# Kernel optimization log

Hardware: AMD Instinct MI355X
Metric: run time of the kernel (lower is better)

Reference implementation:

```python
import jax, jax.numpy as jnp
import numpy as np

B, T, N, E = 64, 500, 21, 210
IN_DIM, HID, OUT_DIM = 1, 128, 1


def gcn_norm(edge_index, edge_weight, num_nodes):
    # PyG gcn_norm: add self loops (weight 1), deg over target nodes, symmetric normalization.
    src, dst = edge_index[0], edge_index[1]
    loop = jnp.arange(num_nodes)
    src = jnp.concatenate([src, loop])
    dst = jnp.concatenate([dst, loop])
    ew = jnp.concatenate([edge_weight, jnp.ones((num_nodes,), edge_weight.dtype)])
    deg = jnp.zeros((num_nodes,), edge_weight.dtype).at[dst].add(ew)
    dinv = jnp.where(deg > 0, deg ** -0.5, 0.0)
    norm = dinv[src] * ew * dinv[dst]
    # Dense N x N (N=21, tiny) normalized adjacency; out[i] = sum_j A[i, j] x[j].
    return jnp.zeros((num_nodes, num_nodes), edge_weight.dtype).at[dst, src].add(norm)


def _forward(edge_index, x, edge_weight, Wz_1, bz_1, lzw_1, lzb_1, Wr_1, br_1, lrw_1, lrb_1, Wh_1, bh_1, lhw_1, lhb_1, Wz_2, bz_2, lzw_2, lzb_2, Wr_2, br_2, lrw_2, lrb_2, Wh_2, bh_2, lhw_2, lhb_2, cls_w, cls_b):
    A = gcn_norm(edge_index, edge_weight, N)

    def gcn(X, W, b):  # X: (B, N, F)
        return jnp.einsum("ij,bjf->bif", A, X @ W) + b

    def cell(X, H, Wz, bz, lzw, lzb, Wr, br, lrw, lrb, Wh, bh, lhw, lhb):
        Z = jax.nn.sigmoid(jnp.concatenate([gcn(X, Wz, bz), H], -1) @ lzw + lzb)
        R = jax.nn.sigmoid(jnp.concatenate([gcn(X, Wr, br), H], -1) @ lrw + lrb)
        Ht = jnp.tanh(jnp.concatenate([gcn(X, Wh, bh), H * R], -1) @ lhw + lhb)
        return Z * H + (1.0 - Z) * Ht

    def step(carry, x_t):  # x_t: (B, N)
        H1, H2 = carry
        X = x_t[..., None]  # (B, N, 1)
        H1 = cell(X, H1, Wz_1, bz_1, lzw_1, lzb_1, Wr_1, br_1, lrw_1, lrb_1, Wh_1, bh_1, lhw_1, lhb_1)
        H2 = cell(H1, H2, Wz_2, bz_2, lzw_2, lzb_2, Wr_2, br_2, lrw_2, lrb_2, Wh_2, bh_2, lhw_2, lhb_2)
        return (H1, H2), H2.mean(axis=1)  # mean over nodes -> (B, HID)

    H0 = jnp.zeros((x.shape[0], N, HID), x.dtype)
    _, outs = jax.lax.scan(step, (H0, H0), jnp.moveaxis(x, 1, 0))  # outs: (T, B, HID)
    seq_out = outs.mean(axis=0)  # mean over time (== mean over nodes then time in original)
    return seq_out @ cls_w + cls_b  # (B, OUT_DIM)


def setup_inputs():
    key = jax.random.key(0)
    ks = list(jax.random.split(key, 20))
    kit = iter(ks)

    def nrm(shape, scale=0.05):
        return jax.random.normal(next(kit), shape, jnp.float32) * scale

    inp = {}
    inp["x"] = jax.random.normal(next(kit), (B, T, N), jnp.float32)
    inp["edge_index"] = jax.random.randint(next(kit), (2, E), 0, N)
    inp["edge_weight"] = jax.random.uniform(next(kit), (E,), jnp.float32)
    for tag, in_dim in (("1", IN_DIM), ("2", HID)):
        for g in "zrh":
            inp[f"W{g}_{tag}"] = nrm((in_dim, HID))
            inp[f"b{g}_{tag}"] = jnp.zeros((HID,), jnp.float32)
            inp[f"l{g}w_{tag}"] = nrm((2 * HID, HID))
            inp[f"l{g}b_{tag}"] = jnp.zeros((HID,), jnp.float32)
    inp["cls_w"] = nrm((HID, OUT_DIM))
    inp["cls_b"] = jnp.zeros((OUT_DIM,), jnp.float32)
    return inp


def reference(x, edge_index, edge_weight, Wz_1, bz_1, lzw_1, lzb_1, Wr_1, br_1, lrw_1, lrb_1, Wh_1, bh_1, lhw_1, lhb_1, Wz_2, bz_2, lzw_2, lzb_2, Wr_2, br_2, lrw_2, lrb_2, Wh_2, bh_2, lhw_2, lhb_2, cls_w, cls_b):
    return _forward(edge_index, x, edge_weight, Wz_1, bz_1, lzw_1, lzb_1, Wr_1, br_1, lrw_1, lrb_1, Wh_1, bh_1, lhw_1, lhb_1, Wz_2, bz_2, lzw_2, lzb_2, Wr_2, br_2, lrw_2, lrb_2, Wh_2, bh_2, lhw_2, lhb_2, cls_w, cls_b)
```

## Files before the change

kernel.cpp:

```cpp
#include <hip/hip_runtime.h>
#include <hip/hip_bf16.h>


#define NN 21
#define NROW 24
#define HID 128
#define TSTEPS 500
#define EDGES 210
#define RPT 6

#define WS_A     0
#define WS_VEC   1600
#define WS_LZR1  3200
#define WS_LH1   36000
#define WS_WE2   52400
#define WS_LZR2  101600
#define WS_LH2   134400
#define WS_FLAGS 150784
#define WS_RING  154880
#define RING_SLOT 3072
#define WS_END   (WS_RING + 64 * 2 * RING_SLOT)

#define WAVE_SYNC() asm volatile("s_waitcnt lgkmcnt(0)" ::: "memory")
#define VM_SYNC()   asm volatile("s_waitcnt vmcnt(0)" ::: "memory")

typedef float v2f __attribute__((ext_vector_type(2)));

__device__ __forceinline__ v2f lo2(float4 w) { v2f v = {w.x, w.y}; return v; }
__device__ __forceinline__ v2f hi2(float4 w) { v2f v = {w.z, w.w}; return v; }
__device__ __forceinline__ void pkf(v2f& acc, float s, v2f w) {
    v2f ss = {s, s};
    acc = __builtin_elementwise_fma(ss, w, acc);
}
__device__ __forceinline__ float sigmoidf(float v) {
    return 1.0f / (1.0f + expf(-v));
}
__device__ __forceinline__ void dc_store(float* p, float v) {
    asm volatile("global_store_dword %0, %1, off sc0 sc1" :: "v"(p), "v"(v) : "memory");
}

__global__ void build_A(const int* __restrict__ ei, const float* __restrict__ ew,
                        float* __restrict__ Aout) {
    __shared__ double deg[NN];
    __shared__ double dinv[NN];
    __shared__ double Asm[NN * NN];
    int t = threadIdx.x;
    for (int k = t; k < NN * NN; k += blockDim.x) Asm[k] = 0.0;
    if (t < NN) deg[t] = 1.0;
    __syncthreads();
    if (t == 0) {
        for (int e = 0; e < EDGES; e++) deg[ei[EDGES + e]] += (double)ew[e];
        for (int i = 0; i < NN; i++) dinv[i] = deg[i] > 0.0 ? 1.0 / sqrt(deg[i]) : 0.0;
        for (int e = 0; e < EDGES; e++) {
            int s = ei[e], d = ei[EDGES + e];
            Asm[d * NN + s] += dinv[s] * (double)ew[e] * dinv[d];
        }
        for (int i = 0; i < NN; i++) Asm[i * NN + i] += dinv[i] * dinv[i];
    }
    __syncthreads();
    for (int k = t; k < NROW * NN; k += blockDim.x)
        Aout[k] = (k < NN * NN) ? (float)Asm[k] : 0.0f;
}

__global__ void init_flags(unsigned* f) {
    int i = blockIdx.x * blockDim.x + threadIdx.x;
    if (i < 4096) f[i] = 0u;
}

__global__ void pack_bot(const float* __restrict__ w0, const float* __restrict__ w1,
                         float4* __restrict__ out, int ngate) {
    int t = blockIdx.x * blockDim.x + threadIdx.x;
    int per_c = ngate * 128;
    int total = 32 * per_c;
    if (t >= total) return;
    int c = t / per_c, rem = t - c * per_c;
    int gate = rem >> 7;
    int r2 = rem & 127;
    int k2 = r2 >> 6;
    int f0 = r2 & 63;
    int k = 4 * c + 2 * k2;
    const float* src = (gate == 0) ? w0 : w1;
    float4 v;
    v.x = src[(128 + k) * 128 + f0];
    v.y = src[(128 + k) * 128 + f0 + 64];
    v.z = src[(128 + k + 1) * 128 + f0];
    v.w = src[(128 + k + 1) * 128 + f0 + 64];
    out[t] = v;
}

__global__ void make_weff2(const float* __restrict__ Wz2, const float* __restrict__ Wr2,
                           const float* __restrict__ Wh2,
                           const float* __restrict__ lzw2, const float* __restrict__ lrw2,
                           const float* __restrict__ lhw2,
                           float4* __restrict__ out) {
    int t = blockIdx.x * blockDim.x + threadIdx.x;
    if (t >= 32 * 384) return;
    int c = t / 384, rem = t - c * 384;
    int g = rem >> 7;
    int r2 = rem & 127;
    int k2 = r2 >> 6;
    int f0 = r2 & 63;
    int k = 4 * c + 2 * k2;
    const float* W = (g == 0) ? Wz2 : (g == 1) ? Wr2 : Wh2;
    const float* L = (g == 0) ? lzw2 : (g == 1) ? lrw2 : lhw2;
    double a0 = 0, a1 = 0, a2 = 0, a3 = 0;
    for (int m = 0; m < 128; m++) {
        double w0 = (double)W[k * 128 + m];
        double w1 = (double)W[(k + 1) * 128 + m];
        a0 += w0 * (double)L[m * 128 + f0];
        a1 += w0 * (double)L[m * 128 + f0 + 64];
        a2 += w1 * (double)L[m * 128 + f0];
        a3 += w1 * (double)L[m * 128 + f0 + 64];
    }
    out[t] = make_float4((float)a0, (float)a1, (float)a2, (float)a3);
}

__global__ void make_vecs(const float* __restrict__ Wz1, const float* __restrict__ Wr1,
                          const float* __restrict__ Wh1,
                          const float* __restrict__ bz1, const float* __restrict__ br1,
                          const float* __restrict__ bh1,
                          const float* __restrict__ lzw1, const float* __restrict__ lrw1,
                          const float* __restrict__ lhw1,
                          const float* __restrict__ lzb1, const float* __restrict__ lrb1,
                          const float* __restrict__ lhb1,
                          const float* __restrict__ bz2, const float* __restrict__ br2,
                          const float* __restrict__ bh2,
                          const float* __restrict__ lzw2, const float* __restrict__ lrw2,
                          const float* __restrict__ lhw2,
                          const float* __restrict__ lzb2, const float* __restrict__ lrb2,
                          const float* __restrict__ lhb2,
                          float* __restrict__ out) {
    int t = blockIdx.x * blockDim.x + threadIdx.x;
    if (t >= 9 * 128) return;
    int v = t >> 7, f = t & 127;
    double acc = 0.0;
    if (v < 3) {
        const float* W = (v == 0) ? Wz1 : (v == 1) ? Wr1 : Wh1;
        const float* L = (v == 0) ? lzw1 : (v == 1) ? lrw1 : lhw1;
        for (int m = 0; m < 128; m++) acc += (double)W[m] * (double)L[m * 128 + f];
    } else if (v < 6) {
        int g = v - 3;
        const float* bb = (g == 0) ? bz1 : (g == 1) ? br1 : bh1;
        const float* L  = (g == 0) ? lzw1 : (g == 1) ? lrw1 : lhw1;
        const float* lb = (g == 0) ? lzb1 : (g == 1) ? lrb1 : lhb1;
        for (int m = 0; m < 128; m++) acc += (double)bb[m] * (double)L[m * 128 + f];
        acc += (double)lb[f];
    } else {
        int g = v - 6;
        const float* bb = (g == 0) ? bz2 : (g == 1) ? br2 : bh2;
        const float* L  = (g == 0) ? lzw2 : (g == 1) ? lrw2 : lhw2;
        const float* lb = (g == 0) ? lzb2 : (g == 1) ? lrb2 : lhb2;
        for (int m = 0; m < 128; m++) acc += (double)bb[m] * (double)L[m * 128 + f];
        acc += (double)lb[f];
    }
    out[t] = (float)acc;
}

__global__ __launch_bounds__(256, 1) void tgcn_split(
    const float* __restrict__ x, float* __restrict__ ws,
    const float* __restrict__ cls_w, const float* __restrict__ cls_b,
    float* __restrict__ out)
{
    const int bid = blockIdx.x;
    const bool roleA = (bid < 64);
    const int b  = bid & 63;
    const int t  = threadIdx.x;
    const int f0 = t & 63;
    const int f1 = f0 + 64;
    const int gw = __builtin_amdgcn_readfirstlane(t >> 6);
    const int iA = gw * RPT;
    const int nreal = (iA + RPT <= NN) ? RPT : (NN - iA);

    unsigned* fwdp  = (unsigned*)(ws + WS_FLAGS) + b * 32;
    unsigned* backp = (unsigned*)(ws + WS_FLAGS) + 2048 + b * 32;
    float* ringB = ws + WS_RING + (size_t)b * (2 * RING_SLOT);

    __shared__ __align__(16) float sH1[2][NROW * HID];
    __shared__ __align__(16) float sHR1[NROW * HID];
    __shared__ __align__(16) float sH1B[NROW * HID];
    __shared__ __align__(16) float sH2[NROW * HID];
    __shared__ __align__(16) float sHR2[NROW * HID];
    __shared__ __align__(16) float sAH[NROW * HID];
    __shared__ float sA[NROW * NN];
    __shared__ float sax[2][NROW];
    __shared__ double sred[4][HID];

    const float*  vecs = ws + WS_VEC;
    const float4* Lzr1 = (const float4*)(ws + WS_LZR1);
    const float4* Lh1  = (const float4*)(ws + WS_LH1);
    const float4* We2  = (const float4*)(ws + WS_WE2);
    const float4* Lzr2 = (const float4*)(ws + WS_LZR2);
    const float4* Lh2  = (const float4*)(ws + WS_LH2);

    const float4* HR1v = (const float4*)sHR1;
    const float4* HR2v = (const float4*)sHR2;
    const float4* AHv  = (const float4*)sAH;
    const float4* H2v  = (const float4*)sH2;

    for (int k = t; k < 2 * NROW * HID; k += 256) ((float*)sH1)[k] = 0.0f;
    for (int k = t; k < NROW * HID; k += 256) {
        sH2[k] = 0.0f; sHR1[k] = 0.0f; sHR2[k] = 0.0f; sAH[k] = 0.0f; sH1B[k] = 0.0f;
    }
    for (int k = t; k < NROW * NN; k += 256) sA[k] = ws[WS_A + k];

    const v2f wz1v = {vecs[f0],        vecs[f1]};
    const v2f wr1v = {vecs[128 + f0],  vecs[128 + f1]};
    const v2f wh1v = {vecs[256 + f0],  vecs[256 + f1]};
    const v2f cz1v = {vecs[384 + f0],  vecs[384 + f1]};
    const v2f cr1v = {vecs[512 + f0],  vecs[512 + f1]};
    const v2f ch1v = {vecs[640 + f0],  vecs[640 + f1]};
    const v2f cz2v = {vecs[768 + f0],  vecs[768 + f1]};
    const v2f cr2v = {vecs[896 + f0],  vecs[896 + f1]};
    const v2f ch2v = {vecs[1024 + f0], vecs[1024 + f1]};

    __syncthreads();

    if (roleA) {
        const float* xb = x + (size_t)b * (TSTEPS * NN);
        if (t < NROW) {
            float a0s = 0.0f, a1s = 0.0f;
            for (int j = 0; j < NN; j++) {
                a0s = fmaf(sA[t * NN + j], xb[j], a0s);
                a1s = fmaf(sA[t * NN + j], xb[NN + j], a1s);
            }
            sax[0][t] = a0s;
            sax[1][t] = a1s;
        }
        __syncthreads();

        for (int s = 0; s < TSTEPS; s++) {
            if (t == 0 && s >= 2) {
                while (__hip_atomic_load(backp, __ATOMIC_RELAXED,
                                         __HIP_MEMORY_SCOPE_AGENT) < (unsigned)(s - 1))
                    __builtin_amdgcn_s_sleep(2);
            }
            __syncthreads();

            {
                const float* H1rd = sH1[(s + 1) & 1];
                float*       H1wr = sH1[s & 1];
                const float4* H1c = (const float4*)H1rd;
                float* g = ringB + (s & 1) * RING_SLOT;
                float axp[RPT];
                #pragma unroll
                for (int r = 0; r < RPT; r++) axp[r] = sax[s & 1][iA + r];
                v2f az[RPT], ar[RPT];
                #pragma unroll
                for (int r = 0; r < RPT; r++) {
                    az[r] = __builtin_elementwise_fma((v2f){axp[r], axp[r]}, wz1v, cz1v);
                    ar[r] = __builtin_elementwise_fma((v2f){axp[r], axp[r]}, wr1v, cr1v);
                }
                #pragma unroll 2
                for (int c = 0; c < 32; ++c) {
                    const float4 wz0 = Lzr1[c * 256 + f0];
                    const float4 wz1 = Lzr1[c * 256 + 64 + f0];
                    const float4 wr0 = Lzr1[c * 256 + 128 + f0];
                    const float4 wr1 = Lzr1[c * 256 + 192 + f0];
                    #pragma unroll
                    for (int r = 0; r < RPT; r++) {
                        const float4 h = H1c[(iA + r) * 32 + c];
                        pkf(az[r], h.x, lo2(wz0)); pkf(az[r], h.y, hi2(wz0));
                        pkf(az[r], h.z, lo2(wz1)); pkf(az[r], h.w, hi2(wz1));
                        pkf(ar[r], h.x, lo2(wr0)); pkf(ar[r], h.y, hi2(wr0));
                        pkf(ar[r], h.z, lo2(wr1)); pkf(ar[r], h.w, hi2(wr1));
                    }
                }
                v2f zg[RPT], h1c[RPT];
                #pragma unroll
                for (int r = 0; r < RPT; r++) {
                    zg[r].x = sigmoidf(az[r].x);
                    zg[r].y = sigmoidf(az[r].y);
                    const float r0 = sigmoidf(ar[r].x);
                    const float r1 = sigmoidf(ar[r].y);
                    h1c[r].x = H1rd[(iA + r) * HID + f0];
                    h1c[r].y = H1rd[(iA + r) * HID + f1];
                    sHR1[(iA + r) * HID + f0] = h1c[r].x * r0;
                    sHR1[(iA + r) * HID + f1] = h1c[r].y * r1;
                }
                WAVE_SYNC();
                v2f ah[RPT];
                #pragma unroll
                for (int r = 0; r < RPT; r++)
                    ah[r] = __builtin_elementwise_fma((v2f){axp[r], axp[r]}, wh1v, ch1v);
                #pragma unroll 2
                for (int c = 0; c < 32; ++c) {
                    const float4 wh0 = Lh1[c * 128 + f0];
                    const float4 wh1 = Lh1[c * 128 + 64 + f0];
                    #pragma unroll
                    for (int r = 0; r < RPT; r++) {
                        const float4 q = HR1v[(iA + r) * 32 + c];
                        pkf(ah[r], q.x, lo2(wh0)); pkf(ah[r], q.y, hi2(wh0));
                        pkf(ah[r], q.z, lo2(wh1)); pkf(ah[r], q.w, hi2(wh1));
                    }
                }
                #pragma unroll
                for (int r = 0; r < RPT; r++) {
                    const int row = iA + r;
                    const float n0 = fmaf(zg[r].x, h1c[r].x, (1.0f - zg[r].x) * tanhf(ah[r].x));
                    const float n1 = fmaf(zg[r].y, h1c[r].y, (1.0f - zg[r].y) * tanhf(ah[r].y));
                    H1wr[row * HID + f0] = n0;
                    H1wr[row * HID + f1] = n1;
                    dc_store(g + row * HID + f0, n0);
                    dc_store(g + row * HID + f1, n1);
                }
            }
            if (t < NROW && s + 2 < TSTEPS) {
                const float* xt = xb + (size_t)(s + 2) * NN;
                float a = 0.0f;
                for (int j = 0; j < NN; j++) a = fmaf(sA[t * NN + j], xt[j], a);
                sax[(s + 2) & 1][t] = a;
            }
            VM_SYNC();
            __syncthreads();
            if (t == 0)
                __hip_atomic_store(fwdp, (unsigned)(s + 1), __ATOMIC_RELAXED,
                                   __HIP_MEMORY_SCOPE_AGENT);
        }
        return;
    }

    double oacc0 = 0.0, oacc1 = 0.0;
    v2f ph[RPT], z2[RPT], h2c[RPT];

    auto l2_p5 = [&]() {
        #pragma unroll 2
        for (int c = 0; c < 32; ++c) {
            const float4 lh0 = Lh2[c * 128 + f0];
            const float4 lh1 = Lh2[c * 128 + 64 + f0];
            #pragma unroll
            for (int r = 0; r < RPT; r++) {
                const float4 q = HR2v[(iA + r) * 32 + c];
                pkf(ph[r], q.x, lo2(lh0)); pkf(ph[r], q.y, hi2(lh0));
                pkf(ph[r], q.z, lo2(lh1)); pkf(ph[r], q.w, hi2(lh1));
            }
        }
        #pragma unroll
        for (int r = 0; r < RPT; r++) {
            const float m0 = fmaf(z2[r].x, h2c[r].x, (1.0f - z2[r].x) * tanhf(ph[r].x));
            const float m1 = fmaf(z2[r].y, h2c[r].y, (1.0f - z2[r].y) * tanhf(ph[r].y));
            sH2[(iA + r) * HID + f0] = m0;
            sH2[(iA + r) * HID + f1] = m1;
            if (r < nreal) {
                oacc0 += (double)m0;
                oacc1 += (double)m1;
            }
        }
    };

    for (int k = 0; k < TSTEPS; k++) {
        if (k >= 1) l2_p5();
        if (t == 0) {
            while (__hip_atomic_load(fwdp, __ATOMIC_RELAXED,
                                     __HIP_MEMORY_SCOPE_AGENT) < (unsigned)(k + 1))
                __builtin_amdgcn_s_sleep(2);
        }
        __syncthreads();
        {
            const float4* gs = (const float4*)(ringB + (k & 1) * RING_SLOT);
            const float4* p0 = gs + t;
            const float4* p1 = gs + t + 256;
            const float4* p2 = gs + t + 512;
            float4 v0, v1, v2;
            asm volatile(
                "global_load_dwordx4 %0, %3, off sc0 sc1\n\t"
                "global_load_dwordx4 %1, %4, off sc0 sc1\n\t"
                "global_load_dwordx4 %2, %5, off sc0 sc1\n\t"
                "s_waitcnt vmcnt(0)"
                : "=v"(v0), "=v"(v1), "=v"(v2)
                : "v"(p0), "v"(p1), "v"(p2)
                : "memory");
            float4* sB = (float4*)sH1B;
            sB[t] = v0; sB[t + 256] = v1; sB[t + 512] = v2;
        }
        WAVE_SYNC();
        __syncthreads();
        if (t == 0)
            __hip_atomic_store(backp, (unsigned)(k + 1), __ATOMIC_RELAXED,
                               __HIP_MEMORY_SCOPE_AGENT);
        {
            v2f aa[RPT];
            #pragma unroll
            for (int r = 0; r < RPT; r++) aa[r] = (v2f){0.0f, 0.0f};
            #pragma unroll 3
            for (int j = 0; j < NN; j++) {
                const v2f hj = {sH1B[j * HID + f0], sH1B[j * HID + f1]};
                #pragma unroll
                for (int r = 0; r < RPT; r++) {
                    const float arj = sA[(iA + r) * NN + j];
                    aa[r] = __builtin_elementwise_fma((v2f){arj, arj}, hj, aa[r]);
                }
            }
            #pragma unroll
            for (int r = 0; r < RPT; r++) {
                sAH[(iA + r) * HID + f0] = aa[r].x;
                sAH[(iA + r) * HID + f1] = aa[r].y;
            }
        }
        WAVE_SYNC();
        {
            v2f pz[RPT], pr[RPT];
            #pragma unroll
            for (int r = 0; r < RPT; r++) { pz[r] = cz2v; pr[r] = cr2v; ph[r] = ch2v; }
            for (int c = 0; c < 32; ++c) {
                const float4 wz0 = We2[c * 384 + f0];
                const float4 wz1 = We2[c * 384 + 64 + f0];
                const float4 wr0 = We2[c * 384 + 128 + f0];
                const float4 wr1 = We2[c * 384 + 192 + f0];
                const float4 wh0 = We2[c * 384 + 256 + f0];
                const float4 wh1 = We2[c * 384 + 320 + f0];
                const float4 lz0 = Lzr2[c * 256 + f0];
                const float4 lz1 = Lzr2[c * 256 + 64 + f0];
                const float4 lr0 = Lzr2[c * 256 + 128 + f0];
                const float4 lr1 = Lzr2[c * 256 + 192 + f0];
                #pragma unroll
                for (int r = 0; r < RPT; r++) {
                    const float4 a = AHv[(iA + r) * 32 + c];
                    const float4 q = H2v[(iA + r) * 32 + c];
                    pkf(pz[r], a.x, lo2(wz0)); pkf(pz[r], a.y, hi2(wz0));
                    pkf(pz[r], a.z, lo2(wz1)); pkf(pz[r], a.w, hi2(wz1));
                    pkf(pz[r], q.x, lo2(lz0)); pkf(pz[r], q.y, hi2(lz0));
                    pkf(pz[r], q.z, lo2(lz1)); pkf(pz[r], q.w, hi2(lz1));
                    pkf(pr[r], a.x, lo2(wr0)); pkf(pr[r], a.y, hi2(wr0));
                    pkf(pr[r], a.z, lo2(wr1)); pkf(pr[r], a.w, hi2(wr1));
                    pkf(pr[r], q.x, lo2(lr0)); pkf(pr[r], q.y, hi2(lr0));
                    pkf(pr[r], q.z, lo2(lr1)); pkf(pr[r], q.w, hi2(lr1));
                    pkf(ph[r], a.x, lo2(wh0)); pkf(ph[r], a.y, hi2(wh0));
                    pkf(ph[r], a.z, lo2(wh1)); pkf(ph[r], a.w, hi2(wh1));
                }
            }
            #pragma unroll
            for (int r = 0; r < RPT; r++) {
                z2[r].x = sigmoidf(pz[r].x);
                z2[r].y = sigmoidf(pz[r].y);
                const float r20 = sigmoidf(pr[r].x);
                const float r21 = sigmoidf(pr[r].y);
                h2c[r].x = sH2[(iA + r) * HID + f0];
                h2c[r].y = sH2[(iA + r) * HID + f1];
                sHR2[(iA + r) * HID + f0] = h2c[r].x * r20;
                sHR2[(iA + r) * HID + f1] = h2c[r].y * r21;
            }
        }
        WAVE_SYNC();
    }

    l2_p5();
    sred[gw][f0] = oacc0;
    sred[gw][f1] = oacc1;
    __syncthreads();
    if (t < HID) {
        double s = 0.0;
        for (int gg = 0; gg < 4; gg++) s += sred[gg][t];
        sred[0][t] = (s / (double)(TSTEPS * NN)) * (double)cls_w[t];
    }
    __syncthreads();
    if (t < 64) {
        double v = ((double*)sred)[t] + ((double*)sred)[t + 64];
        for (int off = 32; off; off >>= 1) v += __shfl_down(v, off, 64);
        if (t == 0) out[b] = (float)(v + (double)cls_b[0]);
    }
}

#define NTHREADS 512
__global__ __launch_bounds__(NTHREADS, 1) void tgcn_main(
    const float* __restrict__ x, const float* __restrict__ ws,
    const float* __restrict__ cls_w, const float* __restrict__ cls_b,
    float* __restrict__ out)
{
    const int b  = blockIdx.x;
    const int t  = threadIdx.x;
    const bool isA = (t < 256);
    const int lt = t & 255;
    const int f0 = lt & 63;
    const int f1 = f0 + 64;
    const int gw = __builtin_amdgcn_readfirstlane(lt >> 6);
    const int iA = gw * RPT;
    const int nreal = (iA + RPT <= NN) ? RPT : (NN - iA);

    __shared__ __align__(16) float sH1[2][NROW * HID];
    __shared__ __align__(16) float sH2[NROW * HID];
    __shared__ __align__(16) float sHR1[NROW * HID];
    __shared__ __align__(16) float sHR2[NROW * HID];
    __shared__ __align__(16) float sAH[NROW * HID];
    __shared__ float sA[NROW * NN];
    __shared__ float sax[2][NROW];
    __shared__ double sred[4][HID];

    const float*  vecs = ws + WS_VEC;
    const float4* Lzr1 = (const float4*)(ws + WS_LZR1);
    const float4* Lh1  = (const float4*)(ws + WS_LH1);
    const float4* We2  = (const float4*)(ws + WS_WE2);
    const float4* Lzr2 = (const float4*)(ws + WS_LZR2);
    const float4* Lh2  = (const float4*)(ws + WS_LH2);

    const float4* H2v  = (const float4*)sH2;
    const float4* HR1v = (const float4*)sHR1;
    const float4* HR2v = (const float4*)sHR2;
    const float4* AHv  = (const float4*)sAH;

    for (int k = t; k < 2 * NROW * HID; k += NTHREADS) ((float*)sH1)[k] = 0.0f;
    for (int k = t; k < NROW * HID; k += NTHREADS) sH2[k] = 0.0f;
    for (int k = t; k < NROW * NN; k += NTHREADS) sA[k] = ws[WS_A + k];

    const v2f wz1v = {vecs[f0],        vecs[f1]};
    const v2f wr1v = {vecs[128 + f0],  vecs[128 + f1]};
    const v2f wh1v = {vecs[256 + f0],  vecs[256 + f1]};
    const v2f cz1v = {vecs[384 + f0],  vecs[384 + f1]};
    const v2f cr1v = {vecs[512 + f0],  vecs[512 + f1]};
    const v2f ch1v = {vecs[640 + f0],  vecs[640 + f1]};
    const v2f cz2v = {vecs[768 + f0],  vecs[768 + f1]};
    const v2f cr2v = {vecs[896 + f0],  vecs[896 + f1]};
    const v2f ch2v = {vecs[1024 + f0], vecs[1024 + f1]};

    __syncthreads();

    const float* xb = x + (size_t)b * (TSTEPS * NN);
    if (t < NROW) {
        float a0s = 0.0f, a1s = 0.0f;
        for (int j = 0; j < NN; j++) {
            a0s = fmaf(sA[t * NN + j], xb[j], a0s);
            a1s = fmaf(sA[t * NN + j], xb[NN + j], a1s);
        }
        sax[0][t] = a0s;
        sax[1][t] = a1s;
    }
    __syncthreads();

    double oacc0 = 0.0, oacc1 = 0.0;

    auto layer1 = [&](int s) {
        const float* H1rd = sH1[(s + 1) & 1];
        float*       H1wr = sH1[s & 1];
        const float4* H1c = (const float4*)H1rd;
        float axp[RPT];
        #pragma unroll
        for (int r = 0; r < RPT; r++) axp[r] = sax[s & 1][iA + r];
        v2f az[RPT], ar[RPT];
        #pragma unroll
        for (int r = 0; r < RPT; r++) {
            az[r] = __builtin_elementwise_fma((v2f){axp[r], axp[r]}, wz1v, cz1v);
            ar[r] = __builtin_elementwise_fma((v2f){axp[r], axp[r]}, wr1v, cr1v);
        }
        #pragma unroll 2
        for (int c = 0; c < 32; ++c) {
            const float4 wz0 = Lzr1[c * 256 + f0];
            const float4 wz1 = Lzr1[c * 256 + 64 + f0];
            const float4 wr0 = Lzr1[c * 256 + 128 + f0];
            const float4 wr1 = Lzr1[c * 256 + 192 + f0];
            #pragma unroll
            for (int r = 0; r < RPT; r++) {
                const float4 h = H1c[(iA + r) * 32 + c];
                pkf(az[r], h.x, lo2(wz0)); pkf(az[r], h.y, hi2(wz0));
                pkf(az[r], h.z, lo2(wz1)); pkf(az[r], h.w, hi2(wz1));
                pkf(ar[r], h.x, lo2(wr0)); pkf(ar[r], h.y, hi2(wr0));
                pkf(ar[r], h.z, lo2(wr1)); pkf(ar[r], h.w, hi2(wr1));
            }
        }
        v2f zg[RPT], h1c[RPT];
        #pragma unroll
        for (int r = 0; r < RPT; r++) {
            zg[r].x = sigmoidf(az[r].x);
            zg[r].y = sigmoidf(az[r].y);
            const float r0 = sigmoidf(ar[r].x);
            const float r1 = sigmoidf(ar[r].y);
            h1c[r].x = H1rd[(iA + r) * HID + f0];
            h1c[r].y = H1rd[(iA + r) * HID + f1];
            sHR1[(iA + r) * HID + f0] = h1c[r].x * r0;
            sHR1[(iA + r) * HID + f1] = h1c[r].y * r1;
        }
        WAVE_SYNC();
        v2f ah[RPT];
        #pragma unroll
        for (int r = 0; r < RPT; r++)
            ah[r] = __builtin_elementwise_fma((v2f){axp[r], axp[r]}, wh1v, ch1v);
        #pragma unroll 2
        for (int c = 0; c < 32; ++c) {
            const float4 wh0 = Lh1[c * 128 + f0];
            const float4 wh1 = Lh1[c * 128 + 64 + f0];
            #pragma unroll
            for (int r = 0; r < RPT; r++) {
                const float4 q = HR1v[(iA + r) * 32 + c];
                pkf(ah[r], q.x, lo2(wh0)); pkf(ah[r], q.y, hi2(wh0));
                pkf(ah[r], q.z, lo2(wh1)); pkf(ah[r], q.w, hi2(wh1));
            }
        }
        #pragma unroll
        for (int r = 0; r < RPT; r++) {
            const float n0 = fmaf(zg[r].x, h1c[r].x, (1.0f - zg[r].x) * tanhf(ah[r].x));
            const float n1 = fmaf(zg[r].y, h1c[r].y, (1.0f - zg[r].y) * tanhf(ah[r].y));
            H1wr[(iA + r) * HID + f0] = n0;
            H1wr[(iA + r) * HID + f1] = n1;
        }
    };

    if (isA) layer1(0);
    __syncthreads();

    for (int k = 0; k < TSTEPS; k++) {
        if (isA) {
            if (k + 1 < TSTEPS) {
                layer1(k + 1);
                if (t < NROW && k + 2 < TSTEPS) {
                    const float* xt = xb + (size_t)(k + 2) * NN;
                    float a = 0.0f;
                    for (int j = 0; j < NN; j++) a = fmaf(sA[t * NN + j], xt[j], a);
                    sax[(k + 2) & 1][t] = a;
                }
            }
        } else {
            const float* H1rd = sH1[k & 1];
            v2f aa[RPT];
            #pragma unroll
            for (int r = 0; r < RPT; r++) aa[r] = (v2f){0.0f, 0.0f};
            #pragma unroll 3
            for (int j = 0; j < NN; j++) {
                const v2f hj = {H1rd[j * HID + f0], H1rd[j * HID + f1]};
                #pragma unroll
                for (int r = 0; r < RPT; r++) {
                    const float arj = sA[(iA + r) * NN + j];
                    aa[r] = __builtin_elementwise_fma((v2f){arj, arj}, hj, aa[r]);
                }
            }
            #pragma unroll
            for (int r = 0; r < RPT; r++) {
                sAH[(iA + r) * HID + f0] = aa[r].x;
                sAH[(iA + r) * HID + f1] = aa[r].y;
            }
            WAVE_SYNC();
            v2f pz[RPT], pr[RPT], ph[RPT];
            #pragma unroll
            for (int r = 0; r < RPT; r++) { pz[r] = cz2v; pr[r] = cr2v; ph[r] = ch2v; }
            for (int c = 0; c < 32; ++c) {
                const float4 wz0 = We2[c * 384 + f0];
                const float4 wz1 = We2[c * 384 + 64 + f0];
                const float4 wr0 = We2[c * 384 + 128 + f0];
                const float4 wr1 = We2[c * 384 + 192 + f0];
                const float4 wh0 = We2[c * 384 + 256 + f0];
                const float4 wh1 = We2[c * 384 + 320 + f0];
                const float4 lz0 = Lzr2[c * 256 + f0];
                const float4 lz1 = Lzr2[c * 256 + 64 + f0];
                const float4 lr0 = Lzr2[c * 256 + 128 + f0];
                const float4 lr1 = Lzr2[c * 256 + 192 + f0];
                #pragma unroll
                for (int r = 0; r < RPT; r++) {
                    const float4 a = AHv[(iA + r) * 32 + c];
                    const float4 q = H2v[(iA + r) * 32 + c];
                    pkf(pz[r], a.x, lo2(wz0)); pkf(pz[r], a.y, hi2(wz0));
                    pkf(pz[r], a.z, lo2(wz1)); pkf(pz[r], a.w, hi2(wz1));
                    pkf(pz[r], q.x, lo2(lz0)); pkf(pz[r], q.y, hi2(lz0));
                    pkf(pz[r], q.z, lo2(lz1)); pkf(pz[r], q.w, hi2(lz1));
                    pkf(pr[r], a.x, lo2(wr0)); pkf(pr[r], a.y, hi2(wr0));
                    pkf(pr[r], a.z, lo2(wr1)); pkf(pr[r], a.w, hi2(wr1));
                    pkf(pr[r], q.x, lo2(lr0)); pkf(pr[r], q.y, hi2(lr0));
                    pkf(pr[r], q.z, lo2(lr1)); pkf(pr[r], q.w, hi2(lr1));
                    pkf(ph[r], a.x, lo2(wh0)); pkf(ph[r], a.y, hi2(wh0));
                    pkf(ph[r], a.z, lo2(wh1)); pkf(ph[r], a.w, hi2(wh1));
                }
            }
            v2f z2[RPT], h2c[RPT];
            #pragma unroll
            for (int r = 0; r < RPT; r++) {
                z2[r].x = sigmoidf(pz[r].x);
                z2[r].y = sigmoidf(pz[r].y);
                const float r20 = sigmoidf(pr[r].x);
                const float r21 = sigmoidf(pr[r].y);
                h2c[r].x = sH2[(iA + r) * HID + f0];
                h2c[r].y = sH2[(iA + r) * HID + f1];
                sHR2[(iA + r) * HID + f0] = h2c[r].x * r20;
                sHR2[(iA + r) * HID + f1] = h2c[r].y * r21;
            }
            WAVE_SYNC();
            #pragma unroll 2
            for (int c = 0; c < 32; ++c) {
                const float4 lh0 = Lh2[c * 128 + f0];
                const float4 lh1 = Lh2[c * 128 + 64 + f0];
                #pragma unroll
                for (int r = 0; r < RPT; r++) {
                    const float4 q = HR2v[(iA + r) * 32 + c];
                    pkf(ph[r], q.x, lo2(lh0)); pkf(ph[r], q.y, hi2(lh0));
                    pkf(ph[r], q.z, lo2(lh1)); pkf(ph[r], q.w, hi2(lh1));
                }
            }
            #pragma unroll
            for (int r = 0; r < RPT; r++) {
                const float m0 = fmaf(z2[r].x, h2c[r].x, (1.0f - z2[r].x) * tanhf(ph[r].x));
                const float m1 = fmaf(z2[r].y, h2c[r].y, (1.0f - z2[r].y) * tanhf(ph[r].y));
                sH2[(iA + r) * HID + f0] = m0;
                sH2[(iA + r) * HID + f1] = m1;
                if (r < nreal) {
                    oacc0 += (double)m0;
                    oacc1 += (double)m1;
                }
            }
        }
        __syncthreads();
    }

    if (!isA) {
        sred[gw][f0] = oacc0;
        sred[gw][f1] = oacc1;
    }
    __syncthreads();
    if (t < HID) {
        double s = 0.0;
        for (int gg = 0; gg < 4; gg++) s += sred[gg][t];
        sred[0][t] = (s / (double)(TSTEPS * NN)) * (double)cls_w[t];
    }
    __syncthreads();
    if (t < 64) {
        double v = ((double*)sred)[t] + ((double*)sred)[t + 64];
        for (int off = 32; off; off >>= 1) v += __shfl_down(v, off, 64);
        if (t == 0) out[b] = (float)(v + (double)cls_b[0]);
    }
}

extern "C" void kernel_launch(void* const* d_in, const int* in_sizes, int n_in,
                              void* d_out, int out_size, void* d_ws, size_t ws_size,
                              hipStream_t stream) {
    const float* x    = (const float*)d_in[0];
    const int*   ei   = (const int*)  d_in[1];
    const float* ew   = (const float*)d_in[2];
    const float* Wz1  = (const float*)d_in[3];
    const float* bz1  = (const float*)d_in[4];
    const float* lzw1 = (const float*)d_in[5];
    const float* lzb1 = (const float*)d_in[6];
    const float* Wr1  = (const float*)d_in[7];
    const float* br1  = (const float*)d_in[8];
    const float* lrw1 = (const float*)d_in[9];
    const float* lrb1 = (const float*)d_in[10];
    const float* Wh1  = (const float*)d_in[11];
    const float* bh1  = (const float*)d_in[12];
    const float* lhw1 = (const float*)d_in[13];
    const float* lhb1 = (const float*)d_in[14];
    const float* Wz2  = (const float*)d_in[15];
    const float* bz2  = (const float*)d_in[16];
    const float* lzw2 = (const float*)d_in[17];
    const float* lzb2 = (const float*)d_in[18];
    const float* Wr2  = (const float*)d_in[19];
    const float* br2  = (const float*)d_in[20];
    const float* lrw2 = (const float*)d_in[21];
    const float* lrb2 = (const float*)d_in[22];
    const float* Wh2  = (const float*)d_in[23];
    const float* bh2  = (const float*)d_in[24];
    const float* lhw2 = (const float*)d_in[25];
    const float* lhb2 = (const float*)d_in[26];
    const float* clsw = (const float*)d_in[27];
    const float* clsb = (const float*)d_in[28];

    float* ws   = (float*)d_ws;
    float* outp = (float*)d_out;

    build_A<<<1, 64, 0, stream>>>(ei, ew, ws + WS_A);
    pack_bot<<<32, 256, 0, stream>>>(lzw1, lrw1, (float4*)(ws + WS_LZR1), 2);
    pack_bot<<<16, 256, 0, stream>>>(lhw1, lhw1, (float4*)(ws + WS_LH1), 1);
    pack_bot<<<32, 256, 0, stream>>>(lzw2, lrw2, (float4*)(ws + WS_LZR2), 2);
    pack_bot<<<16, 256, 0, stream>>>(lhw2, lhw2, (float4*)(ws + WS_LH2), 1);
    make_weff2<<<48, 256, 0, stream>>>(Wz2, Wr2, Wh2, lzw2, lrw2, lhw2,
                                       (float4*)(ws + WS_WE2));
    make_vecs<<<5, 256, 0, stream>>>(Wz1, Wr1, Wh1, bz1, br1, bh1,
                                     lzw1, lrw1, lhw1, lzb1, lrb1, lhb1,
                                     bz2, br2, bh2, lzw2, lrw2, lhw2,
                                     lzb2, lrb2, lhb2, ws + WS_VEC);

    const size_t need = (size_t)WS_END * sizeof(float);
    if (ws_size >= need) {
        init_flags<<<16, 256, 0, stream>>>((unsigned*)(ws + WS_FLAGS));
        tgcn_split<<<128, 256, 0, stream>>>(x, ws, clsw, clsb, outp);
    } else {
        tgcn_main<<<64, NTHREADS, 0, stream>>>(x, ws, clsw, clsb, outp);
    }
}
```

Before: 10.08 ms.

## Deepen producer-consumer ring and prefetch next H1 slot during layer-2 compute

The global ring buffer between the layer-1 producer blocks and the layer-2 consumer blocks now holds up to four slots when the workspace allows it, so the producer can run further ahead. The consumer double-buffers the received H1 in shared memory, issues the global loads for step k+1 before the layer-2 gate matmuls, and waits on them only afterwards. This is meant to hide the cross-block handoff and global load latency behind compute. The cost is extra LDS for the second H1 buffer, more live registers during the gate loop, and a larger workspace requirement.

Result: no change. 10.06 ms, median of 2 (-0.2%).

```diff
diff --git a/kernel.cpp b/kernel.cpp
--- a/kernel.cpp
+++ b/kernel.cpp
@@ -19,7 +19,6 @@
 #define WS_FLAGS 150784
 #define WS_RING  154880
 #define RING_SLOT 3072
-#define WS_END   (WS_RING + 64 * 2 * RING_SLOT)
 
 #define WAVE_SYNC() asm volatile("s_waitcnt lgkmcnt(0)" ::: "memory")
 #define VM_SYNC()   asm volatile("s_waitcnt vmcnt(0)" ::: "memory")
@@ -159,7 +158,7 @@
 __global__ __launch_bounds__(256, 1) void tgcn_split(
     const float* __restrict__ x, float* __restrict__ ws,
     const float* __restrict__ cls_w, const float* __restrict__ cls_b,
-    float* __restrict__ out)
+    float* __restrict__ out, int rdepth)
 {
     const int bid = blockIdx.x;
     const bool roleA = (bid < 64);
@@ -170,14 +169,15 @@
     const int gw = __builtin_amdgcn_readfirstlane(t >> 6);
     const int iA = gw * RPT;
     const int nreal = (iA + RPT <= NN) ? RPT : (NN - iA);
+    const int dmask = rdepth - 1;
 
     unsigned* fwdp  = (unsigned*)(ws + WS_FLAGS) + b * 32;
     unsigned* backp = (unsigned*)(ws + WS_FLAGS) + 2048 + b * 32;
-    float* ringB = ws + WS_RING + (size_t)b * (2 * RING_SLOT);
+    float* ringB = ws + WS_RING + (size_t)b * ((size_t)rdepth * RING_SLOT);
 
     __shared__ __align__(16) float sH1[2][NROW * HID];
     __shared__ __align__(16) float sHR1[NROW * HID];
-    __shared__ __align__(16) float sH1B[NROW * HID];
+    __shared__ __align__(16) float sH1B[2][NROW * HID];
     __shared__ __align__(16) float sH2[NROW * HID];
     __shared__ __align__(16) float sHR2[NROW * HID];
     __shared__ __align__(16) float sAH[NROW * HID];
@@ -197,9 +197,12 @@
     const float4* AHv  = (const float4*)sAH;
     const float4* H2v  = (const float4*)sH2;
 
-    for (int k = t; k < 2 * NROW * HID; k += 256) ((float*)sH1)[k] = 0.0f;
+    for (int k = t; k < 2 * NROW * HID; k += 256) {
+        ((float*)sH1)[k] = 0.0f;
+        ((float*)sH1B)[k] = 0.0f;
+    }
     for (int k = t; k < NROW * HID; k += 256) {
-        sH2[k] = 0.0f; sHR1[k] = 0.0f; sHR2[k] = 0.0f; sAH[k] = 0.0f; sH1B[k] = 0.0f;
+        sH2[k] = 0.0f; sHR1[k] = 0.0f; sHR2[k] = 0.0f; sAH[k] = 0.0f;
     }
     for (int k = t; k < NROW * NN; k += 256) sA[k] = ws[WS_A + k];
 
@@ -229,9 +232,9 @@
         __syncthreads();
 
         for (int s = 0; s < TSTEPS; s++) {
-            if (t == 0 && s >= 2) {
+            if (t == 0 && s >= rdepth) {
                 while (__hip_atomic_load(backp, __ATOMIC_RELAXED,
-                                         __HIP_MEMORY_SCOPE_AGENT) < (unsigned)(s - 1))
+                                         __HIP_MEMORY_SCOPE_AGENT) < (unsigned)(s - rdepth + 1))
                     __builtin_amdgcn_s_sleep(2);
             }
             __syncthreads();
@@ -240,7 +243,7 @@
                 const float* H1rd = sH1[(s + 1) & 1];
                 float*       H1wr = sH1[s & 1];
                 const float4* H1c = (const float4*)H1rd;
-                float* g = ringB + (s & 1) * RING_SLOT;
+                float* g = ringB + (s & dmask) * RING_SLOT;
                 float axp[RPT];
                 #pragma unroll
                 for (int r = 0; r < RPT; r++) axp[r] = sax[s & 1][iA + r];
@@ -347,56 +350,77 @@
         }
     };
 
-    for (int k = 0; k < TSTEPS; k++) {
-        if (k >= 1) l2_p5();
+    {
         if (t == 0) {
             while (__hip_atomic_load(fwdp, __ATOMIC_RELAXED,
-                                     __HIP_MEMORY_SCOPE_AGENT) < (unsigned)(k + 1))
+                                     __HIP_MEMORY_SCOPE_AGENT) < 1u)
                 __builtin_amdgcn_s_sleep(2);
         }
         __syncthreads();
+        const float4* gs = (const float4*)(ringB + 0 * RING_SLOT);
+        const float4* p0 = gs + t;
+        const float4* p1 = gs + t + 256;
+        const float4* p2 = gs + t + 512;
+        float4 v0, v1, v2;
+        asm volatile(
+            "global_load_dwordx4 %0, %3, off sc0 sc1\n\t"
+            "global_load_dwordx4 %1, %4, off sc0 sc1\n\t"
+            "global_load_dwordx4 %2, %5, off sc0 sc1\n\t"
+            "s_waitcnt vmcnt(0)"
+            : "=v"(v0), "=v"(v1), "=v"(v2)
+            : "v"(p0), "v"(p1), "v"(p2)
+            : "memory");
+        float4* sB = (float4*)sH1B[0];
+        sB[t] = v0; sB[t + 256] = v1; sB[t + 512] = v2;
+        __syncthreads();
+        if (t == 0)
+            __hip_atomic_store(backp, 1u, __ATOMIC_RELAXED,
+                               __HIP_MEMORY_SCOPE_AGENT);
+    }
+
+    for (int k = 0; k < TSTEPS; k++) {
+        const float* H1k = sH1B[k & 1];
         {
-            const float4* gs = (const float4*)(ringB + (k & 1) * RING_SLOT);
+            v2f aa[RPT];
+            #pragma unroll
+            for (int r = 0; r < RPT; r++) aa[r] = (v2f){0.0f, 0.0f};
+            #pragma unroll 3
+            for (int j = 0; j < NN; j++) {
+                const v2f hj = {H1k[j * HID + f0], H1k[j * HID + f1]};
+                #pragma unroll
+                for (int r = 0; r < RPT; r++) {
+                    const float arj = sA[(iA + r) * NN + j];
+                    aa[r] = __builtin_elementwise_fma((v2f){arj, arj}, hj, aa[r]);
+                }
+            }
+            #pragma unroll
+            for (int r = 0; r < RPT; r++) {
+                sAH[(iA + r) * HID + f0] = aa[r].x;
+                sAH[(iA + r) * HID + f1] = aa[r].y;
+            }
+        }
+        WAVE_SYNC();
+        const bool pf = (k + 1 < TSTEPS);
+        float4 v0, v1, v2;
+        if (pf) {
+            if (t == 0) {
+                while (__hip_atomic_load(fwdp, __ATOMIC_RELAXED,
+                                         __HIP_MEMORY_SCOPE_AGENT) < (unsigned)(k + 2))
+                    __builtin_amdgcn_s_sleep(2);
+            }
+            __syncthreads();
+            const float4* gs = (const float4*)(ringB + ((k + 1) & dmask) * RING_SLOT);
             const float4* p0 = gs + t;
             const float4* p1 = gs + t + 256;
             const float4* p2 = gs + t + 512;
-            float4 v0, v1, v2;
             asm volatile(
                 "global_load_dwordx4 %0, %3, off sc0 sc1\n\t"
                 "global_load_dwordx4 %1, %4, off sc0 sc1\n\t"
-                "global_load_dwordx4 %2, %5, off sc0 sc1\n\t"
-                "s_waitcnt vmcnt(0)"
+                "global_load_dwordx4 %2, %5, off sc0 sc1"
                 : "=v"(v0), "=v"(v1), "=v"(v2)
                 : "v"(p0), "v"(p1), "v"(p2)
                 : "memory");
-            float4* sB = (float4*)sH1B;
-            sB[t] = v0; sB[t + 256] = v1; sB[t + 512] = v2;
-        }
-        WAVE_SYNC();
-        __syncthreads();
-        if (t == 0)
-            __hip_atomic_store(backp, (unsigned)(k + 1), __ATOMIC_RELAXED,
-                               __HIP_MEMORY_SCOPE_AGENT);
-        {
-            v2f aa[RPT];
-            #pragma unroll
-            for (int r = 0; r < RPT; r++) aa[r] = (v2f){0.0f, 0.0f};
-            #pragma unroll 3
-            for (int j = 0; j < NN; j++) {
-                const v2f hj = {sH1B[j * HID + f0], sH1B[j * HID + f1]};
-                #pragma unroll
-                for (int r = 0; r < RPT; r++) {
-                    const float arj = sA[(iA + r) * NN + j];
-                    aa[r] = __builtin_elementwise_fma((v2f){arj, arj}, hj, aa[r]);
-                }
-            }
-            #pragma unroll
-            for (int r = 0; r < RPT; r++) {
-                sAH[(iA + r) * HID + f0] = aa[r].x;
-                sAH[(iA + r) * HID + f1] = aa[r].y;
-            }
-        }
-        WAVE_SYNC();
+        }
         {
             v2f pz[RPT], pr[RPT];
             #pragma unroll
@@ -441,9 +465,19 @@
             }
         }
         WAVE_SYNC();
-    }
-
-    l2_p5();
+        if (pf) {
+            asm volatile("s_waitcnt vmcnt(0)" ::: "memory");
+            __builtin_amdgcn_sched_barrier(0);
+            float4* sB = (float4*)sH1B[(k + 1) & 1];
+            sB[t] = v0; sB[t + 256] = v1; sB[t + 512] = v2;
+            __syncthreads();
+            if (t == 0)
+                __hip_atomic_store(backp, (unsigned)(k + 2), __ATOMIC_RELAXED,
+                                   __HIP_MEMORY_SCOPE_AGENT);
+        }
+        l2_p5();
+    }
+
     sred[gw][f0] = oacc0;
     sred[gw][f1] = oacc1;
     __syncthreads();
@@ -761,10 +795,15 @@
                                      bz2, br2, bh2, lzw2, lrw2, lhw2,
                                      lzb2, lrb2, lhb2, ws + WS_VEC);
 
-    const size_t need = (size_t)WS_END * sizeof(float);
-    if (ws_size >= need) {
+    const size_t need4 = (size_t)(WS_RING + 64 * 4 * RING_SLOT) * sizeof(float);
+    const size_t need2 = (size_t)(WS_RING + 64 * 2 * RING_SLOT) * sizeof(float);
+    int rdepth = 0;
+    if (ws_size >= need4)      rdepth = 4;
+    else if (ws_size >= need2) rdepth = 2;
+
+    if (rdepth) {
         init_flags<<<16, 256, 0, stream>>>((unsigned*)(ws + WS_FLAGS));
-        tgcn_split<<<128, 256, 0, stream>>>(x, ws, clsw, clsb, outp);
+        tgcn_split<<<128, 256, 0, stream>>>(x, ws, clsw, clsb, outp, rdepth);
     } else {
         tgcn_main<<<64, NTHREADS, 0, stream>>>(x, ws, clsw, clsb, outp);
     }
```
